# Kernel tuning notes

Hardware: AMD Instinct MI355X
Metric: run time of the kernel (lower is better)

## Reference

```python
import jax, jax.numpy as jnp
import numpy as np

TEMPERATURE = 0.01
VMIN, VMAX = -1.0, 1.0
NUM_VALUES = 256


def setup_inputs() -> dict:
    key = jax.random.key(0)
    k_img, k_cmap = jax.random.split(key)
    image = jax.random.uniform(k_img, (4, 3, 512, 512), dtype=jnp.float32)
    cmap = jax.random.uniform(k_cmap, (NUM_VALUES, 3), dtype=jnp.float32)
    idx = jnp.arange(NUM_VALUES, dtype=jnp.float32)
    v_i = VMIN + (VMAX - VMIN) * idx / (NUM_VALUES - 1)
    return {"image": image, "cmap": cmap, "v_i": v_i}


def reference(image, cmap, v_i):
    # image: (N, 3, H, W) -> (N, H, W, 3)
    img = jnp.transpose(image, (0, 2, 3, 1))
    # squared euclidean distance to each of the 256 colormap colors
    # dist[n,h,w,k] = sum_c (img[n,h,w,c] - cmap[k,c])^2
    diff = img[..., None, :] - cmap  # (N, H, W, K, 3)
    distances = jnp.sum(diff * diff, axis=-1)  # (N, H, W, K)
    weights = jax.nn.softmax(-distances / TEMPERATURE, axis=-1)
    velocities = jnp.einsum('nhwk,k->nhw', weights, v_i)
    return velocities
```

## Files before the change

kernel.cpp:

```cpp
#include <hip/hip_runtime.h>
#include <hip/hip_fp16.h>


typedef __attribute__((ext_vector_type(8))) short short8;
typedef __attribute__((ext_vector_type(8))) _Float16 f16x8;
typedef __attribute__((ext_vector_type(4))) float f32x4;

#define HWSZ 262144
#define NPIX 1048576
#define K2F  144.2695040888963f
#define BIASF 14.0f
#define PXB  256

static __device__ __forceinline__ unsigned f2bf(float x, float* resid) {
  unsigned u = __builtin_bit_cast(unsigned, x);
  unsigned r = (u + 0x7fffu + ((u >> 16) & 1u)) >> 16;
  if (resid) *resid = x - __builtin_bit_cast(float, r << 16);
  return r;
}
static __device__ __forceinline__ unsigned bfp(unsigned lo, unsigned hi) {
  return (lo & 0xffffu) | (hi << 16);
}
static __device__ __forceinline__ unsigned pkrtz(float a, float b) {
  return __builtin_bit_cast(unsigned, __builtin_amdgcn_cvt_pkrtz(a, b));
}

__global__ __launch_bounds__(512, 8) void rgb2vel_main(
    const float* __restrict__ img, const float* __restrict__ cmap,
    const float* __restrict__ vv, float* __restrict__ out) {
  __shared__ __align__(16) int4 sA4[PXB * 5];
  __shared__ __align__(16) int4 sB4[1024];
  __shared__ __align__(16) int4 sBv4[512];
  const int tid = threadIdx.x;
  const int lane = tid & 63;
  const int warp = tid >> 6;
  const int c = lane & 15;
  const int g = lane >> 4;
  const int pb0 = blockIdx.x * PXB;

  if (tid < 256) {
    int k = tid;
    float c0 = cmap[k * 3 + 0], c1 = cmap[k * 3 + 1], c2 = cmap[k * 3 + 2];
    float cc[3] = {c0, c1, c2};
    unsigned H[3], M[3], L[3];
    float r;
#pragma unroll
    for (int ch = 0; ch < 3; ++ch) {
      float x = 2.0f * K2F * cc[ch];
      H[ch] = f2bf(x, &r);
      M[ch] = f2bf(r, &r);
      L[ch] = f2bf(r, nullptr);
    }
    float mcc = BIASF - K2F * (c0 * c0 + c1 * c1 + c2 * c2);
    unsigned mh = f2bf(mcc, &r);
    unsigned mm = f2bf(r, &r);
    unsigned ml = f2bf(r, nullptr);
    const unsigned N1 = 0xBF80u;
    unsigned d[16];
    d[0] = bfp(H[0], H[1]); d[1] = bfp(H[2], H[0]); d[2] = bfp(H[1], H[2]);
    d[3] = bfp(M[0], M[1]); d[4] = bfp(M[2], L[0]); d[5] = bfp(L[1], L[2]);
    d[6] = bfp(M[0], M[1]); d[7] = bfp(M[2], H[0]); d[8] = bfp(H[1], H[2]);
    d[9] = bfp(mh, mm);     d[10] = bfp(ml, N1);    d[11] = bfp(N1, N1);
    d[12] = d[13] = d[14] = d[15] = 0u;
    int col = k & 15, tt = k >> 4;
#pragma unroll
    for (int g2 = 0; g2 < 4; ++g2)
      sB4[tt * 64 + g2 * 16 + col] =
          make_int4((int)d[4 * g2 + 0], (int)d[4 * g2 + 1],
                    (int)d[4 * g2 + 2], (int)d[4 * g2 + 3]);
  } else {
    int px = tid - 256;
    int idx = pb0 + px;
    int n = idx >> 18;
    int hw = idx & (HWSZ - 1);
    const float* pbp = img + (size_t)n * 3 * HWSZ + hw;
    float p0 = pbp[0], p1 = pbp[HWSZ], p2 = pbp[2 * HWSZ];
    float pc[3] = {p0, p1, p2};
    unsigned ph[3], pm[3], pl[3];
    float r;
#pragma unroll
    for (int ch = 0; ch < 3; ++ch) {
      ph[ch] = f2bf(pc[ch], &r);
      pm[ch] = f2bf(r, &r);
      pl[ch] = f2bf(r, nullptr);
    }
    float qv = K2F * (p0 * p0 + p1 * p1 + p2 * p2);
    unsigned qh = f2bf(qv, &r);
    unsigned qm = f2bf(r, &r);
    unsigned ql = f2bf(r, nullptr);
    const unsigned ONE = 0x3F80u;
    int4* sb = &sA4[px * 5];
    sb[0] = make_int4((int)bfp(ph[0], ph[1]), (int)bfp(ph[2], pm[0]),
                      (int)bfp(pm[1], pm[2]), (int)bfp(ph[0], ph[1]));
    sb[1] = make_int4((int)bfp(ph[2], ph[0]), (int)bfp(ph[1], ph[2]),
                      (int)bfp(pm[0], pm[1]), (int)bfp(pm[2], pl[0]));
    sb[2] = make_int4((int)bfp(pl[1], pl[2]), (int)bfp(ONE, ONE),
                      (int)bfp(ONE, qh),      (int)bfp(qm, ql));
    sb[3] = make_int4(0, 0, 0, 0);
  }

  {
    int u = tid >> 6, l = tid & 63, cc2 = l & 15, gg = l >> 4;
    int4 q = make_int4(0, 0, 0, 0);
    if (cc2 == 0) {
      q = make_int4(0x3C003C00, 0x3C003C00, 0x3C003C00, 0x3C003C00);
    } else if (cc2 == 1) {
      unsigned hq[4];
#pragma unroll
      for (int jp = 0; jp < 4; ++jp) {
        int j0 = 2 * jp, j1 = 2 * jp + 1;
        int i0 = (2 * u + (j0 >> 2)) * 16 + gg * 4 + (j0 & 3);
        int i1 = (2 * u + (j1 >> 2)) * 16 + gg * 4 + (j1 & 3);
        unsigned h0 = (unsigned)__half_as_ushort(__float2half(vv[i0]));
        unsigned h1 = (unsigned)__half_as_ushort(__float2half(vv[i1]));
        hq[jp] = h0 | (h1 << 16);
      }
      q = make_int4((int)hq[0], (int)hq[1], (int)hq[2], (int)hq[3]);
    }
    sBv4[tid] = q;
  }
  __syncthreads();

  short8 pfr0 = __builtin_bit_cast(short8, sA4[(warp * 16 + c) * 5 + g]);
  short8 pfr1 = __builtin_bit_cast(short8, sA4[(128 + warp * 16 + c) * 5 + g]);

  f32x4 accA = {0.f, 0.f, 0.f, 0.f};
  f32x4 accB = {0.f, 0.f, 0.f, 0.f};
  const f32x4 z = {0.f, 0.f, 0.f, 0.f};

#pragma unroll
  for (int u = 0; u < 8; ++u) {
    short8 ca = __builtin_bit_cast(short8, sB4[(2 * u) * 64 + lane]);
    short8 cb = __builtin_bit_cast(short8, sB4[(2 * u + 1) * 64 + lane]);
    f32x4 d0a = __builtin_amdgcn_mfma_f32_16x16x32_bf16(ca, pfr0, z, 0, 0, 0);
    f32x4 d1a = __builtin_amdgcn_mfma_f32_16x16x32_bf16(cb, pfr0, z, 0, 0, 0);
    f32x4 d0b = __builtin_amdgcn_mfma_f32_16x16x32_bf16(ca, pfr1, z, 0, 0, 0);
    f32x4 d1b = __builtin_amdgcn_mfma_f32_16x16x32_bf16(cb, pfr1, z, 0, 0, 0);
    union { unsigned w[4]; f16x8 v8; } wa, wb;
    wa.w[0] = pkrtz(__builtin_amdgcn_exp2f(d0a[0]), __builtin_amdgcn_exp2f(d0a[1]));
    wa.w[1] = pkrtz(__builtin_amdgcn_exp2f(d0a[2]), __builtin_amdgcn_exp2f(d0a[3]));
    wa.w[2] = pkrtz(__builtin_amdgcn_exp2f(d1a[0]), __builtin_amdgcn_exp2f(d1a[1]));
    wa.w[3] = pkrtz(__builtin_amdgcn_exp2f(d1a[2]), __builtin_amdgcn_exp2f(d1a[3]));
    wb.w[0] = pkrtz(__builtin_amdgcn_exp2f(d0b[0]), __builtin_amdgcn_exp2f(d0b[1]));
    wb.w[1] = pkrtz(__builtin_amdgcn_exp2f(d0b[2]), __builtin_amdgcn_exp2f(d0b[3]));
    wb.w[2] = pkrtz(__builtin_amdgcn_exp2f(d1b[0]), __builtin_amdgcn_exp2f(d1b[1]));
    wb.w[3] = pkrtz(__builtin_amdgcn_exp2f(d1b[2]), __builtin_amdgcn_exp2f(d1b[3]));
    f16x8 bv = __builtin_bit_cast(f16x8, sBv4[u * 64 + lane]);
    accA = __builtin_amdgcn_mfma_f32_16x16x32_f16(wa.v8, bv, accA, 0, 0, 0);
    accB = __builtin_amdgcn_mfma_f32_16x16x32_f16(wb.v8, bv, accB, 0, 0, 0);
  }

  float a0 = __shfl_xor(accA[0], 1);
  float a1 = __shfl_xor(accA[1], 1);
  float a2 = __shfl_xor(accA[2], 1);
  float a3 = __shfl_xor(accA[3], 1);
  float b0 = __shfl_xor(accB[0], 1);
  float b1 = __shfl_xor(accB[1], 1);
  float b2 = __shfl_xor(accB[2], 1);
  float b3 = __shfl_xor(accB[3], 1);
  if (c == 0) {
    float* oA = out + pb0 + warp * 16 + g * 4;
    oA[0] = a0 * __builtin_amdgcn_rcpf(accA[0]);
    oA[1] = a1 * __builtin_amdgcn_rcpf(accA[1]);
    oA[2] = a2 * __builtin_amdgcn_rcpf(accA[2]);
    oA[3] = a3 * __builtin_amdgcn_rcpf(accA[3]);
    float* oB = out + pb0 + 128 + warp * 16 + g * 4;
    oB[0] = b0 * __builtin_amdgcn_rcpf(accB[0]);
    oB[1] = b1 * __builtin_amdgcn_rcpf(accB[1]);
    oB[2] = b2 * __builtin_amdgcn_rcpf(accB[2]);
    oB[3] = b3 * __builtin_amdgcn_rcpf(accB[3]);
  }
}

extern "C" void kernel_launch(void* const* d_in, const int* in_sizes, int n_in,
                              void* d_out, int out_size, void* d_ws, size_t ws_size,
                              hipStream_t stream) {
  const float* image = (const float*)d_in[0];
  const float* cmap  = (const float*)d_in[1];
  const float* v_i   = (const float*)d_in[2];
  float* out = (float*)d_out;

  rgb2vel_main<<<NPIX / PXB, 512, 0, stream>>>(image, cmap, v_i, out);
}
```

Measured before the change: 95.54 us.

## Make kernel persistent with prefetch of next pixel tile across generations

Launches a fixed grid of 512 blocks, each processing 8 pixel tiles in a loop. The colormap and velocity tables are staged into shared memory once per block instead of once per tile. The next tile's image values are loaded into registers before the MFMA/exp loop and written to shared memory after it, so global load latency overlaps with compute. This adds two block barriers per tile and lowers the occupancy hint to 4.

```diff
diff --git a/kernel.cpp b/kernel.cpp
--- a/kernel.cpp
+++ b/kernel.cpp
@@ -11,6 +11,8 @@
 #define K2F  144.2695040888963f
 #define BIASF 14.0f
 #define PXB  256
+#define GRID 512
+#define GENS 8
 
 static __device__ __forceinline__ unsigned f2bf(float x, float* resid) {
   unsigned u = __builtin_bit_cast(unsigned, x);
@@ -25,7 +27,32 @@
   return __builtin_bit_cast(unsigned, __builtin_amdgcn_cvt_pkrtz(a, b));
 }
 
-__global__ __launch_bounds__(512, 8) void rgb2vel_main(
+static __device__ __forceinline__ void stage_px(float p0, float p1, float p2,
+                                                int4* sb) {
+  float pc[3] = {p0, p1, p2};
+  unsigned ph[3], pm[3], pl[3];
+  float r;
+#pragma unroll
+  for (int ch = 0; ch < 3; ++ch) {
+    ph[ch] = f2bf(pc[ch], &r);
+    pm[ch] = f2bf(r, &r);
+    pl[ch] = f2bf(r, nullptr);
+  }
+  float qv = K2F * (p0 * p0 + p1 * p1 + p2 * p2);
+  unsigned qh = f2bf(qv, &r);
+  unsigned qm = f2bf(r, &r);
+  unsigned ql = f2bf(r, nullptr);
+  const unsigned ONE = 0x3F80u;
+  sb[0] = make_int4((int)bfp(ph[0], ph[1]), (int)bfp(ph[2], pm[0]),
+                    (int)bfp(pm[1], pm[2]), (int)bfp(ph[0], ph[1]));
+  sb[1] = make_int4((int)bfp(ph[2], ph[0]), (int)bfp(ph[1], ph[2]),
+                    (int)bfp(pm[0], pm[1]), (int)bfp(pm[2], pl[0]));
+  sb[2] = make_int4((int)bfp(pl[1], pl[2]), (int)bfp(ONE, ONE),
+                    (int)bfp(ONE, qh),      (int)bfp(qm, ql));
+  sb[3] = make_int4(0, 0, 0, 0);
+}
+
+__global__ __launch_bounds__(512, 4) void rgb2vel_main(
     const float* __restrict__ img, const float* __restrict__ cmap,
     const float* __restrict__ vv, float* __restrict__ out) {
   __shared__ __align__(16) int4 sA4[PXB * 5];
@@ -36,7 +63,7 @@
   const int warp = tid >> 6;
   const int c = lane & 15;
   const int g = lane >> 4;
-  const int pb0 = blockIdx.x * PXB;
+  const int bid = blockIdx.x;
 
   if (tid < 256) {
     int k = tid;
@@ -70,33 +97,11 @@
                     (int)d[4 * g2 + 2], (int)d[4 * g2 + 3]);
   } else {
     int px = tid - 256;
-    int idx = pb0 + px;
+    int idx = bid * PXB + px;
     int n = idx >> 18;
     int hw = idx & (HWSZ - 1);
     const float* pbp = img + (size_t)n * 3 * HWSZ + hw;
-    float p0 = pbp[0], p1 = pbp[HWSZ], p2 = pbp[2 * HWSZ];
-    float pc[3] = {p0, p1, p2};
-    unsigned ph[3], pm[3], pl[3];
-    float r;
-#pragma unroll
-    for (int ch = 0; ch < 3; ++ch) {
-      ph[ch] = f2bf(pc[ch], &r);
-      pm[ch] = f2bf(r, &r);
-      pl[ch] = f2bf(r, nullptr);
-    }
-    float qv = K2F * (p0 * p0 + p1 * p1 + p2 * p2);
-    unsigned qh = f2bf(qv, &r);
-    unsigned qm = f2bf(r, &r);
-    unsigned ql = f2bf(r, nullptr);
-    const unsigned ONE = 0x3F80u;
-    int4* sb = &sA4[px * 5];
-    sb[0] = make_int4((int)bfp(ph[0], ph[1]), (int)bfp(ph[2], pm[0]),
-                      (int)bfp(pm[1], pm[2]), (int)bfp(ph[0], ph[1]));
-    sb[1] = make_int4((int)bfp(ph[2], ph[0]), (int)bfp(ph[1], ph[2]),
-                      (int)bfp(pm[0], pm[1]), (int)bfp(pm[2], pl[0]));
-    sb[2] = make_int4((int)bfp(pl[1], pl[2]), (int)bfp(ONE, ONE),
-                      (int)bfp(ONE, qh),      (int)bfp(qm, ql));
-    sb[3] = make_int4(0, 0, 0, 0);
+    stage_px(pbp[0], pbp[HWSZ], pbp[2 * HWSZ], &sA4[px * 5]);
   }
 
   {
@@ -121,54 +126,72 @@
   }
   __syncthreads();
 
-  short8 pfr0 = __builtin_bit_cast(short8, sA4[(warp * 16 + c) * 5 + g]);
-  short8 pfr1 = __builtin_bit_cast(short8, sA4[(128 + warp * 16 + c) * 5 + g]);
-
-  f32x4 accA = {0.f, 0.f, 0.f, 0.f};
-  f32x4 accB = {0.f, 0.f, 0.f, 0.f};
+  float np0 = 0.f, np1 = 0.f, np2 = 0.f;
   const f32x4 z = {0.f, 0.f, 0.f, 0.f};
-
-#pragma unroll
-  for (int u = 0; u < 8; ++u) {
-    short8 ca = __builtin_bit_cast(short8, sB4[(2 * u) * 64 + lane]);
-    short8 cb = __builtin_bit_cast(short8, sB4[(2 * u + 1) * 64 + lane]);
-    f32x4 d0a = __builtin_amdgcn_mfma_f32_16x16x32_bf16(ca, pfr0, z, 0, 0, 0);
-    f32x4 d1a = __builtin_amdgcn_mfma_f32_16x16x32_bf16(cb, pfr0, z, 0, 0, 0);
-    f32x4 d0b = __builtin_amdgcn_mfma_f32_16x16x32_bf16(ca, pfr1, z, 0, 0, 0);
-    f32x4 d1b = __builtin_amdgcn_mfma_f32_16x16x32_bf16(cb, pfr1, z, 0, 0, 0);
-    union { unsigned w[4]; f16x8 v8; } wa, wb;
-    wa.w[0] = pkrtz(__builtin_amdgcn_exp2f(d0a[0]), __builtin_amdgcn_exp2f(d0a[1]));
-    wa.w[1] = pkrtz(__builtin_amdgcn_exp2f(d0a[2]), __builtin_amdgcn_exp2f(d0a[3]));
-    wa.w[2] = pkrtz(__builtin_amdgcn_exp2f(d1a[0]), __builtin_amdgcn_exp2f(d1a[1]));
-    wa.w[3] = pkrtz(__builtin_amdgcn_exp2f(d1a[2]), __builtin_amdgcn_exp2f(d1a[3]));
-    wb.w[0] = pkrtz(__builtin_amdgcn_exp2f(d0b[0]), __builtin_amdgcn_exp2f(d0b[1]));
-    wb.w[1] = pkrtz(__builtin_amdgcn_exp2f(d0b[2]), __builtin_amdgcn_exp2f(d0b[3]));
-    wb.w[2] = pkrtz(__builtin_amdgcn_exp2f(d1b[0]), __builtin_amdgcn_exp2f(d1b[1]));
-    wb.w[3] = pkrtz(__builtin_amdgcn_exp2f(d1b[2]), __builtin_amdgcn_exp2f(d1b[3]));
-    f16x8 bv = __builtin_bit_cast(f16x8, sBv4[u * 64 + lane]);
-    accA = __builtin_amdgcn_mfma_f32_16x16x32_f16(wa.v8, bv, accA, 0, 0, 0);
-    accB = __builtin_amdgcn_mfma_f32_16x16x32_f16(wb.v8, bv, accB, 0, 0, 0);
-  }
-
-  float a0 = __shfl_xor(accA[0], 1);
-  float a1 = __shfl_xor(accA[1], 1);
-  float a2 = __shfl_xor(accA[2], 1);
-  float a3 = __shfl_xor(accA[3], 1);
-  float b0 = __shfl_xor(accB[0], 1);
-  float b1 = __shfl_xor(accB[1], 1);
-  float b2 = __shfl_xor(accB[2], 1);
-  float b3 = __shfl_xor(accB[3], 1);
-  if (c == 0) {
-    float* oA = out + pb0 + warp * 16 + g * 4;
-    oA[0] = a0 * __builtin_amdgcn_rcpf(accA[0]);
-    oA[1] = a1 * __builtin_amdgcn_rcpf(accA[1]);
-    oA[2] = a2 * __builtin_amdgcn_rcpf(accA[2]);
-    oA[3] = a3 * __builtin_amdgcn_rcpf(accA[3]);
-    float* oB = out + pb0 + 128 + warp * 16 + g * 4;
-    oB[0] = b0 * __builtin_amdgcn_rcpf(accB[0]);
-    oB[1] = b1 * __builtin_amdgcn_rcpf(accB[1]);
-    oB[2] = b2 * __builtin_amdgcn_rcpf(accB[2]);
-    oB[3] = b3 * __builtin_amdgcn_rcpf(accB[3]);
+#pragma unroll 1
+  for (int gen = 0; gen < GENS; ++gen) {
+    short8 pfr0 = __builtin_bit_cast(short8, sA4[(warp * 16 + c) * 5 + g]);
+    short8 pfr1 = __builtin_bit_cast(short8, sA4[(128 + warp * 16 + c) * 5 + g]);
+
+    if (tid >= 256 && gen + 1 < GENS) {
+      int idx = (bid + GRID * (gen + 1)) * PXB + (tid - 256);
+      int n = idx >> 18;
+      int hw = idx & (HWSZ - 1);
+      const float* pbp = img + (size_t)n * 3 * HWSZ + hw;
+      np0 = pbp[0];
+      np1 = pbp[HWSZ];
+      np2 = pbp[2 * HWSZ];
+    }
+    __syncthreads();
+
+    f32x4 accA = z, accB = z;
+#pragma unroll
+    for (int u = 0; u < 8; ++u) {
+      short8 ca = __builtin_bit_cast(short8, sB4[(2 * u) * 64 + lane]);
+      short8 cb = __builtin_bit_cast(short8, sB4[(2 * u + 1) * 64 + lane]);
+      f32x4 d0a = __builtin_amdgcn_mfma_f32_16x16x32_bf16(ca, pfr0, z, 0, 0, 0);
+      f32x4 d1a = __builtin_amdgcn_mfma_f32_16x16x32_bf16(cb, pfr0, z, 0, 0, 0);
+      f32x4 d0b = __builtin_amdgcn_mfma_f32_16x16x32_bf16(ca, pfr1, z, 0, 0, 0);
+      f32x4 d1b = __builtin_amdgcn_mfma_f32_16x16x32_bf16(cb, pfr1, z, 0, 0, 0);
+      union { unsigned w[4]; f16x8 v8; } wa, wb;
+      wa.w[0] = pkrtz(__builtin_amdgcn_exp2f(d0a[0]), __builtin_amdgcn_exp2f(d0a[1]));
+      wa.w[1] = pkrtz(__builtin_amdgcn_exp2f(d0a[2]), __builtin_amdgcn_exp2f(d0a[3]));
+      wa.w[2] = pkrtz(__builtin_amdgcn_exp2f(d1a[0]), __builtin_amdgcn_exp2f(d1a[1]));
+      wa.w[3] = pkrtz(__builtin_amdgcn_exp2f(d1a[2]), __builtin_amdgcn_exp2f(d1a[3]));
+      wb.w[0] = pkrtz(__builtin_amdgcn_exp2f(d0b[0]), __builtin_amdgcn_exp2f(d0b[1]));
+      wb.w[1] = pkrtz(__builtin_amdgcn_exp2f(d0b[2]), __builtin_amdgcn_exp2f(d0b[3]));
+      wb.w[2] = pkrtz(__builtin_amdgcn_exp2f(d1b[0]), __builtin_amdgcn_exp2f(d1b[1]));
+      wb.w[3] = pkrtz(__builtin_amdgcn_exp2f(d1b[2]), __builtin_amdgcn_exp2f(d1b[3]));
+      f16x8 bv = __builtin_bit_cast(f16x8, sBv4[u * 64 + lane]);
+      accA = __builtin_amdgcn_mfma_f32_16x16x32_f16(wa.v8, bv, accA, 0, 0, 0);
+      accB = __builtin_amdgcn_mfma_f32_16x16x32_f16(wb.v8, bv, accB, 0, 0, 0);
+    }
+
+    if (tid >= 256 && gen + 1 < GENS)
+      stage_px(np0, np1, np2, &sA4[(tid - 256) * 5]);
+
+    float a0 = __shfl_xor(accA[0], 1);
+    float a1 = __shfl_xor(accA[1], 1);
+    float a2 = __shfl_xor(accA[2], 1);
+    float a3 = __shfl_xor(accA[3], 1);
+    float b0 = __shfl_xor(accB[0], 1);
+    float b1 = __shfl_xor(accB[1], 1);
+    float b2 = __shfl_xor(accB[2], 1);
+    float b3 = __shfl_xor(accB[3], 1);
+    if (c == 0) {
+      int pb0 = (bid + GRID * gen) * PXB;
+      float* oA = out + pb0 + warp * 16 + g * 4;
+      oA[0] = a0 * __builtin_amdgcn_rcpf(accA[0]);
+      oA[1] = a1 * __builtin_amdgcn_rcpf(accA[1]);
+      oA[2] = a2 * __builtin_amdgcn_rcpf(accA[2]);
+      oA[3] = a3 * __builtin_amdgcn_rcpf(accA[3]);
+      float* oB = out + pb0 + 128 + warp * 16 + g * 4;
+      oB[0] = b0 * __builtin_amdgcn_rcpf(accB[0]);
+      oB[1] = b1 * __builtin_amdgcn_rcpf(accB[1]);
+      oB[2] = b2 * __builtin_amdgcn_rcpf(accB[2]);
+      oB[3] = b3 * __builtin_amdgcn_rcpf(accB[3]);
+    }
+    __syncthreads();
   }
 }
 
@@ -180,5 +203,5 @@
   const float* v_i   = (const float*)d_in[2];
   float* out = (float*)d_out;
 
-  rgb2vel_main<<<NPIX / PXB, 512, 0, stream>>>(image, cmap, v_i, out);
-}
+  rgb2vel_main<<<GRID, 512, 0, stream>>>(image, cmap, v_i, out);
+}
```

Result: no change. 96.41 us (+0.9%).
